# Kernel optimization log

Hardware: AMD Instinct MI355X
Metric: run time of the kernel (lower is better)

## Reference

```python
import jax, jax.numpy as jnp
import numpy as np

MAX_EMBED = 1024
MAX_HEADS = 16
MIN_WIDTH_RATIO = 0.25


def setup_inputs() -> dict:
    key = jax.random.key(0)
    ks = jax.random.split(key, 10)
    B, S, E = 4, 1024, MAX_EMBED
    query = jax.random.normal(ks[0], (B, S, E), dtype=jnp.float32)
    attention_mask = jax.random.randint(ks[1], (B, 1, 1, S), 0, 2, dtype=jnp.int32)
    # SlimmableLinear params (max sizes); kaiming-ish scale ~ 1/sqrt(fan_in)
    scale = 1.0 / np.sqrt(E)
    def lin(kw, kb):
        w = jax.random.uniform(kw, (E, E), dtype=jnp.float32, minval=-scale, maxval=scale)
        b = jax.random.uniform(kb, (E,), dtype=jnp.float32, minval=-scale, maxval=scale)
        return w, b
    q_w, q_b = lin(ks[2], ks[3])
    k_w, k_b = lin(ks[4], ks[5])
    v_w, v_b = lin(ks[6], ks[7])
    o_w, o_b = lin(ks[8], ks[9])
    return {"query": query, "attention_mask": attention_mask,
            "q_w": q_w, "q_b": q_b, "k_w": k_w, "k_b": k_b,
            "v_w": v_w, "v_b": v_b, "o_w": o_w, "o_b": o_b,
            "width": 768}


def _slim_linear(x, w, b, width):
    # weight stored [out, in] like torch; slice to [width, width]
    return x[..., :width] @ w[:width, :width].T + b[:width]


def reference(query, attention_mask, q_w, q_b, k_w, k_b, v_w, v_b, o_w, o_b, width):
    min_width = int(MAX_EMBED * MIN_WIDTH_RATIO)
    width = max(min_width, min(int(width), MAX_EMBED))
    num_heads = max(1, width * MAX_HEADS // MAX_EMBED)
    head_dim = width // num_heads
    B, S, _ = query.shape

    q = _slim_linear(query, q_w, q_b, width)  # [B,S,width]
    k = _slim_linear(query, k_w, k_b, width)  # key=query (self-attn)
    v = _slim_linear(query, v_w, v_b, width)

    q = q.reshape(B, S, num_heads, head_dim).transpose(0, 2, 1, 3)  # [B,H,S,D]
    k = k.reshape(B, S, num_heads, head_dim).transpose(0, 2, 1, 3)
    v = v.reshape(B, S, num_heads, head_dim).transpose(0, 2, 1, 3)

    scores = jnp.einsum('bhqd,bhkd->bhqk', q, k) / jnp.sqrt(jnp.float32(head_dim))
    scores = jnp.where(attention_mask == 0, jnp.float32(-1e9), scores)
    attn_weights = jax.nn.softmax(scores, axis=-1)  # [B,H,S,S]
    attn_output = jnp.einsum('bhqk,bhkd->bhqd', attn_weights, v)
    attn_output = attn_output.transpose(0, 2, 1, 3).reshape(B, S, width)
    output = attn_output @ o_w[:width, :width].T + o_b[:width]
    return output, attn_weights
```

## Files before the change

kernel.cpp:

```cpp
#include <hip/hip_runtime.h>

#define Bn 4
#define Sn 1024
#define En 1024
#define Wn 768
#define Hn 12
#define Dn 64
#define XE ((size_t)Bn * Sn * Wn)

typedef __attribute__((ext_vector_type(8))) short short8;
typedef __attribute__((ext_vector_type(4))) short short4v;
typedef __attribute__((ext_vector_type(4))) float floatx4;

#define MFMA16(A, B, C) __builtin_amdgcn_mfma_f32_16x16x32_bf16(A, B, C, 0, 0, 0)

__device__ __forceinline__ unsigned short f2bf_rn(float f) {
    unsigned int u = __float_as_uint(f);
    unsigned int r = u + 0x7fffu + ((u >> 16) & 1u);
    return (unsigned short)(r >> 16);
}
__device__ __forceinline__ float bf2f(unsigned short h) {
    return __uint_as_float(((unsigned int)h) << 16);
}

__device__ __forceinline__ void gload_lds16(const unsigned short* g, unsigned short* l) {
    __builtin_amdgcn_global_load_lds(
        (const __attribute__((address_space(1))) void*)g,
        (__attribute__((address_space(3))) void*)l, 16, 0, 0);
}

__global__ __launch_bounds__(256) void prep_kernel(
    const float* __restrict__ x,
    const float* __restrict__ qw, const float* __restrict__ kw,
    const float* __restrict__ vw, const float* __restrict__ ow,
    const float* __restrict__ qb, const float* __restrict__ kb,
    const float* __restrict__ vb,
    unsigned short* __restrict__ xh, unsigned short* __restrict__ xl,
    unsigned short* __restrict__ wqh, unsigned short* __restrict__ wql,
    unsigned short* __restrict__ woh, unsigned short* __restrict__ wol,
    float* __restrict__ bq)
{
    const int bx = blockIdx.x;
    const float* src; unsigned short *dh, *dl; int e;
    bool lo = true;
    if (bx < 3072) {
        e = (bx * 256 + threadIdx.x) * 4;
        src = x; dh = xh; dl = xl; lo = false;
    } else if (bx < 3072 + 1728) {
        int bb = bx - 3072; int which = bb / 576;
        e = ((bb - which * 576) * 256 + threadIdx.x) * 4;
        src = (which == 0) ? qw : (which == 1) ? kw : vw;
        dh = wqh + (size_t)which * Wn * Wn;
        dl = wql + (size_t)which * Wn * Wn;
    } else if (bx < 3072 + 1728 + 576) {
        e = ((bx - 3072 - 1728) * 256 + threadIdx.x) * 4;
        src = ow; dh = woh; dl = wol;
    } else {
        int t = (bx - 3072 - 1728 - 576) * 256 + threadIdx.x;
        if (t < Wn) bq[t] = qb[t];
        else if (t < 2 * Wn) bq[t] = kb[t - Wn];
        else if (t < 3 * Wn) bq[t] = vb[t - 2 * Wn];
        return;
    }
    int row = e / Wn, col = e - row * Wn;
    float4 v = *(const float4*)(src + (size_t)row * En + col);
    float f[4] = {v.x, v.y, v.z, v.w};
    short4v h, l;
    #pragma unroll
    for (int i = 0; i < 4; ++i) {
        unsigned short hh = f2bf_rn(f[i]);
        h[i] = (short)hh;
        l[i] = (short)f2bf_rn(f[i] - bf2f(hh));
    }
    *(short4v*)(dh + e) = h;
    if (lo) *(short4v*)(dl + e) = l;
}

__global__ __launch_bounds__(256) void qkv_mfma_kernel(
    const unsigned short* __restrict__ xh,
    const unsigned short* __restrict__ wh, const unsigned short* __restrict__ wl,
    const float* __restrict__ bq,
    unsigned short* __restrict__ qh_o, unsigned short* __restrict__ kh_o,
    unsigned short* __restrict__ vt_o)
{
    __shared__ __align__(16) unsigned short Ah[128 * 32];
    __shared__ __align__(16) unsigned short Bh[128 * 32];
    __shared__ __align__(16) unsigned short Bl[128 * 32];

    const int tid = threadIdx.x;
    const int wave = tid >> 6, lane = tid & 63;
    const int quad = lane >> 4, l16 = lane & 15;
    const int yy = ((int)blockIdx.y + 12) % 18;
    const int m0 = blockIdx.x * 128, n0 = yy * 128;
    const int wm = wave >> 1, wn = wave & 1;
    const int which = n0 / Wn;
    const bool full = (which == 2);

    floatx4 acc[4][4] = {};

    const int r_in = lane >> 2;
    const int cs = (lane & 3) ^ (r_in & 3);

    for (int k0 = 0; k0 < Wn; k0 += 32) {
        if (wave == 0) {
            #pragma unroll
            for (int i = 0; i < 8; ++i)
                gload_lds16(xh + (size_t)(m0 + i * 16 + r_in) * Wn + k0 + cs * 8,
                            Ah + i * 512);
        } else if (wave == 1) {
            #pragma unroll
            for (int i = 0; i < 8; ++i)
                gload_lds16(wh + (size_t)(n0 + i * 16 + r_in) * Wn + k0 + cs * 8,
                            Bh + i * 512);
        } else if (wave == 2 && full) {
            #pragma unroll
            for (int i = 0; i < 8; ++i)
                gload_lds16(wl + (size_t)(n0 + i * 16 + r_in) * Wn + k0 + cs * 8,
                            Bl + i * 512);
        }
        __syncthreads();

        short8 afh[4], bfh[4], bfl[4];
        #pragma unroll
        for (int t = 0; t < 4; ++t) {
            int mr = wm * 64 + t * 16 + l16;
            int ca = quad ^ (mr & 3);
            afh[t] = *(const short8*)(Ah + mr * 32 + ca * 8);
            int nr = wn * 64 + t * 16 + l16;
            int cb = quad ^ (nr & 3);
            bfh[t] = *(const short8*)(Bh + nr * 32 + cb * 8);
            if (full) bfl[t] = *(const short8*)(Bl + nr * 32 + cb * 8);
        }
        #pragma unroll
        for (int mt = 0; mt < 4; ++mt)
            #pragma unroll
            for (int nt = 0; nt < 4; ++nt) {
                acc[mt][nt] = MFMA16(afh[mt], bfh[nt], acc[mt][nt]);
                if (full) acc[mt][nt] = MFMA16(afh[mt], bfl[nt], acc[mt][nt]);
            }
        __syncthreads();
    }

    const int b = m0 >> 10;
    #pragma unroll
    for (int nt = 0; nt < 4; ++nt) {
        const int ng = n0 + wn * 64 + nt * 16 + l16;
        const float bias = bq[ng];
        const int f = ng - which * Wn;
        const int h = f >> 6, d = f & 63;
        #pragma unroll
        for (int mt = 0; mt < 4; ++mt) {
            const int mbase = m0 + wm * 64 + mt * 16 + quad * 4;
            const int s0 = mbase & (Sn - 1);
            if (which < 2) {
                unsigned short* oq = which ? kh_o : qh_o;
                size_t idx = (((size_t)(b * Hn + h)) * Sn + s0) * Dn + d;
                #pragma unroll
                for (int r = 0; r < 4; ++r)
                    oq[idx + (size_t)r * Dn] = f2bf_rn(acc[mt][nt][r] + bias);
            } else {
                size_t idx = (((size_t)(b * Hn + h)) * Dn + d) * Sn + s0;
                short4v pk;
                #pragma unroll
                for (int r = 0; r < 4; ++r)
                    pk[r] = (short)f2bf_rn(acc[mt][nt][r] + bias);
                *(short4v*)(vt_o + idx) = pk;
            }
        }
    }
}

__global__ __launch_bounds__(256) void attn_fused_kernel(
    const unsigned short* __restrict__ qh, const unsigned short* __restrict__ kh,
    const unsigned short* __restrict__ vt, const int* __restrict__ mask,
    float* __restrict__ attn,
    unsigned short* __restrict__ aoh, unsigned short* __restrict__ aol)
{
    __shared__ __align__(16) char PsObuf[3 * 16 * 68 * 4];
    __shared__ float msk[Sn];
    __shared__ float Lsum[4][16];

    unsigned short (*Ps)[16 * 72] =
        (unsigned short (*)[16 * 72])PsObuf;
    float (*Obuf)[16][68] = (float (*)[16][68])PsObuf;

    const int tid = threadIdx.x;
    const int wave = tid >> 6, lane = tid & 63;
    const int quad = lane >> 4, l16 = lane & 15;
    const int qt = blockIdx.x;
    const int h = blockIdx.y, b = blockIdx.z;
    const int bh = b * Hn + h;
    const size_t kvb = (size_t)bh * Sn * Dn;
    const size_t vbase = (size_t)bh * Dn * Sn;

    {
        int4 mi = *(const int4*)(mask + b * Sn + tid * 4);
        msk[tid * 4 + 0] = (float)mi.x;
        msk[tid * 4 + 1] = (float)mi.y;
        msk[tid * 4 + 2] = (float)mi.z;
        msk[tid * 4 + 3] = (float)mi.w;
    }

    const int qrow = qt * 16 + l16;
    short8 qf[2];
    {
        const unsigned short* qp = qh + kvb + (size_t)qrow * Dn + quad * 8;
        qf[0] = *(const short8*)(qp);
        qf[1] = *(const short8*)(qp + 32);
    }
    __syncthreads();

    short8 Pr[8];
    float lsumr[4] = {0.f, 0.f, 0.f, 0.f};
    const int kbase = wave * 256;

    #pragma unroll
    for (int kk = 0; kk < 4; ++kk) {
        const int k0 = kbase + kk * 64;
        #pragma unroll
        for (int ct = 0; ct < 4; ++ct) {
            const int key = k0 + ct * 16 + l16;
            const unsigned short* kp = kh + kvb + (size_t)key * Dn + quad * 8;
            short8 kf0 = *(const short8*)(kp);
            short8 kf1 = *(const short8*)(kp + 32);
            floatx4 acc = {0.f, 0.f, 0.f, 0.f};
            acc = MFMA16(qf[0], kf0, acc);
            acc = MFMA16(qf[1], kf1, acc);
            const float mv = msk[key];
            #pragma unroll
            for (int r = 0; r < 4; ++r) {
                const float e = __expf(acc[r] * 0.125f) * mv;
                lsumr[r] += e;
                Ps[wave][(quad * 4 + r) * 72 + ct * 16 + l16] = f2bf_rn(e);
            }
        }
        Pr[kk * 2 + 0] = *(const short8*)&Ps[wave][l16 * 72 + quad * 8];
        Pr[kk * 2 + 1] = *(const short8*)&Ps[wave][l16 * 72 + 32 + quad * 8];
    }

    #pragma unroll
    for (int r = 0; r < 4; ++r) {
        float v = lsumr[r];
        v += __shfl_xor(v, 1, 64);
        v += __shfl_xor(v, 2, 64);
        v += __shfl_xor(v, 4, 64);
        v += __shfl_xor(v, 8, 64);
        lsumr[r] = v;
    }
    if (l16 == 0) {
        #pragma unroll
        for (int r = 0; r < 4; ++r) Lsum[wave][quad * 4 + r] = lsumr[r];
    }
    __syncthreads();

    float li[4];
    #pragma unroll
    for (int r = 0; r < 4; ++r) {
        const float lv = Lsum[0][quad * 4 + r] + Lsum[1][quad * 4 + r]
                       + Lsum[2][quad * 4 + r] + Lsum[3][quad * 4 + r];
        li[r] = (lv > 0.f) ? 1.f / lv : 0.f;
    }
    float lt;
    {
        const float lv = Lsum[0][l16] + Lsum[1][l16] + Lsum[2][l16] + Lsum[3][l16];
        lt = (lv > 0.f) ? 1.f / lv : 0.f;
    }

    floatx4 oacc[4] = {};
    float* aprow = attn + ((size_t)bh * Sn + qrow) * Sn;

    #pragma unroll
    for (int kk = 0; kk < 4; ++kk) {
        const int k0 = kbase + kk * 64;
        #pragma unroll
        for (int ksp = 0; ksp < 2; ++ksp) {
            const short8 pf = Pr[kk * 2 + ksp];
            float4 f0, f1;
            f0.x = bf2f((unsigned short)pf[0]) * lt;
            f0.y = bf2f((unsigned short)pf[1]) * lt;
            f0.z = bf2f((unsigned short)pf[2]) * lt;
            f0.w = bf2f((unsigned short)pf[3]) * lt;
            f1.x = bf2f((unsigned short)pf[4]) * lt;
            f1.y = bf2f((unsigned short)pf[5]) * lt;
            f1.z = bf2f((unsigned short)pf[6]) * lt;
            f1.w = bf2f((unsigned short)pf[7]) * lt;
            float* ap = aprow + k0 + ksp * 32 + quad * 8;
            *(float4*)(ap)     = f0;
            *(float4*)(ap + 4) = f1;
            #pragma unroll
            for (int dt = 0; dt < 4; ++dt) {
                short8 vf = *(const short8*)(vt + vbase
                              + (size_t)(dt * 16 + l16) * Sn + k0 + ksp * 32 + quad * 8);
                oacc[dt] = MFMA16(pf, vf, oacc[dt]);
            }
        }
    }

    if (wave != 0) {
        #pragma unroll
        for (int dt = 0; dt < 4; ++dt)
            #pragma unroll
            for (int r = 0; r < 4; ++r)
                Obuf[wave - 1][quad * 4 + r][dt * 16 + l16] = oacc[dt][r];
    }
    __syncthreads();
    if (wave == 0) {
        const int row0 = qt * 16 + quad * 4;
        #pragma unroll
        for (int dt = 0; dt < 4; ++dt)
            #pragma unroll
            for (int r = 0; r < 4; ++r) {
                const float o = (oacc[dt][r]
                               + Obuf[0][quad * 4 + r][dt * 16 + l16]
                               + Obuf[1][quad * 4 + r][dt * 16 + l16]
                               + Obuf[2][quad * 4 + r][dt * 16 + l16]) * li[r];
                const unsigned short hh = f2bf_rn(o);
                const size_t idx = ((size_t)b * Sn + row0 + r) * Wn + h * Dn + dt * 16 + l16;
                aoh[idx] = hh;
                aol[idx] = f2bf_rn(o - bf2f(hh));
            }
    }
}

__global__ __launch_bounds__(256) void oproj_mfma_kernel(
    const unsigned short* __restrict__ aoh, const unsigned short* __restrict__ aol,
    const unsigned short* __restrict__ wh, const unsigned short* __restrict__ wl,
    const float* __restrict__ ob, float* __restrict__ out)
{
    __shared__ __align__(16) unsigned short Ah[64 * 32];
    __shared__ __align__(16) unsigned short Al[64 * 32];
    __shared__ __align__(16) unsigned short Bh[128 * 32];
    __shared__ __align__(16) unsigned short Bl[128 * 32];

    const int tid = threadIdx.x;
    const int wave = tid >> 6, lane = tid & 63;
    const int quad = lane >> 4, l16 = lane & 15;
    const int m0 = blockIdx.x * 64, n0 = blockIdx.y * 128;
    const int wm = wave >> 1, wn = wave & 1;

    floatx4 acc[2][4] = {};

    const int r_in = lane >> 2;
    const int cs = (lane & 3) ^ (r_in & 3);

    for (int k0 = 0; k0 < Wn; k0 += 32) {
        if (wave == 0) {
            #pragma unroll
            for (int i = 0; i < 4; ++i) {
                gload_lds16(aoh + (size_t)(m0 + i * 16 + r_in) * Wn + k0 + cs * 8,
                            Ah + i * 512);
                gload_lds16(aol + (size_t)(m0 + i * 16 + r_in) * Wn + k0 + cs * 8,
                            Al + i * 512);
            }
        } else if (wave == 1) {
            #pragma unroll
            for (int i = 0; i < 8; ++i)
                gload_lds16(wh + (size_t)(n0 + i * 16 + r_in) * Wn + k0 + cs * 8,
                            Bh + i * 512);
        } else if (wave == 2) {
            #pragma unroll
            for (int i = 0; i < 8; ++i)
                gload_lds16(wl + (size_t)(n0 + i * 16 + r_in) * Wn + k0 + cs * 8,
                            Bl + i * 512);
        }
        __syncthreads();

        short8 afh[2], afl[2], bfh[4], bfl[4];
        #pragma unroll
        for (int t = 0; t < 2; ++t) {
            int mr = wm * 32 + t * 16 + l16;
            int ca = quad ^ (mr & 3);
            afh[t] = *(const short8*)(Ah + mr * 32 + ca * 8);
            afl[t] = *(const short8*)(Al + mr * 32 + ca * 8);
        }
        #pragma unroll
        for (int t = 0; t < 4; ++t) {
            int nr = wn * 64 + t * 16 + l16;
            int cb = quad ^ (nr & 3);
            bfh[t] = *(const short8*)(Bh + nr * 32 + cb * 8);
            bfl[t] = *(const short8*)(Bl + nr * 32 + cb * 8);
        }
        #pragma unroll
        for (int mt = 0; mt < 2; ++mt)
            #pragma unroll
            for (int nt = 0; nt < 4; ++nt) {
                acc[mt][nt] = MFMA16(afh[mt], bfh[nt], acc[mt][nt]);
                acc[mt][nt] = MFMA16(afh[mt], bfl[nt], acc[mt][nt]);
                acc[mt][nt] = MFMA16(afl[mt], bfh[nt], acc[mt][nt]);
            }
        __syncthreads();
    }

    #pragma unroll
    for (int nt = 0; nt < 4; ++nt) {
        const int ng = n0 + wn * 64 + nt * 16 + l16;
        const float bias = ob[ng];
        #pragma unroll
        for (int mt = 0; mt < 2; ++mt) {
            const int m = m0 + wm * 32 + mt * 16 + quad * 4;
            #pragma unroll
            for (int r = 0; r < 4; ++r)
                out[(size_t)(m + r) * Wn + ng] = acc[mt][nt][r] + bias;
        }
    }
}

extern "C" void kernel_launch(void* const* d_in, const int* in_sizes, int n_in,
                              void* d_out, int out_size, void* d_ws, size_t ws_size,
                              hipStream_t stream) {
    const float* x    = (const float*)d_in[0];
    const int*   mask = (const int*)  d_in[1];
    const float* qw = (const float*)d_in[2];
    const float* qb = (const float*)d_in[3];
    const float* kw = (const float*)d_in[4];
    const float* kb = (const float*)d_in[5];
    const float* vw = (const float*)d_in[6];
    const float* vb = (const float*)d_in[7];
    const float* ow = (const float*)d_in[8];
    const float* ob = (const float*)d_in[9];

    float* out  = (float*)d_out;
    float* attn = out + XE;

    char* w = (char*)d_ws;
    unsigned short* xh   = (unsigned short*)w;  w += XE * 2;
    unsigned short* xl   = (unsigned short*)w;  w += XE * 2;
    unsigned short* wqh  = (unsigned short*)w;  w += (size_t)3 * Wn * Wn * 2;
    unsigned short* wql  = (unsigned short*)w;  w += (size_t)3 * Wn * Wn * 2;
    unsigned short* woh  = (unsigned short*)w;  w += (size_t)Wn * Wn * 2;
    unsigned short* wol  = (unsigned short*)w;  w += (size_t)Wn * Wn * 2;
    float*          bq   = (float*)w;           w += (size_t)3 * Wn * 4;
    unsigned short* qh   = (unsigned short*)w;  w += XE * 2;
    unsigned short* kh   = (unsigned short*)w;  w += XE * 2;
    unsigned short* vt_w = (unsigned short*)w;  w += XE * 2;

    prep_kernel<<<5385, 256, 0, stream>>>(x, qw, kw, vw, ow, qb, kb, vb,
                                          xh, xl, wqh, wql, woh, wol, bq);

    qkv_mfma_kernel<<<dim3(32, 18), 256, 0, stream>>>(
        xh, wqh, wql, bq, qh, kh, vt_w);

    attn_fused_kernel<<<dim3(64, Hn, Bn), 256, 0, stream>>>(
        qh, kh, vt_w, mask, attn, xh, xl);

    oproj_mfma_kernel<<<dim3(64, 6), 256, 0, stream>>>(
        xh, xl, woh, wol, ob, out);
}
```

Measured before the change: 384.1 us.

## Stage attention-prob stores through LDS and drop low-bf16 split for O-projection input

Result: faster. 374.4 us (-2.5%).

```diff
diff --git a/kernel.cpp b/kernel.cpp
--- a/kernel.cpp
+++ b/kernel.cpp
@@ -52,6 +52,7 @@
         src = (which == 0) ? qw : (which == 1) ? kw : vw;
         dh = wqh + (size_t)which * Wn * Wn;
         dl = wql + (size_t)which * Wn * Wn;
+        lo = (which == 2);
     } else if (bx < 3072 + 1728 + 576) {
         e = ((bx - 3072 - 1728) * 256 + threadIdx.x) * 4;
         src = ow; dh = woh; dl = wol;
@@ -173,15 +174,15 @@
 __global__ __launch_bounds__(256) void attn_fused_kernel(
     const unsigned short* __restrict__ qh, const unsigned short* __restrict__ kh,
     const unsigned short* __restrict__ vt, const int* __restrict__ mask,
-    float* __restrict__ attn,
-    unsigned short* __restrict__ aoh, unsigned short* __restrict__ aol)
+    float* __restrict__ attn, unsigned short* __restrict__ aoh)
 {
-    __shared__ __align__(16) char PsObuf[3 * 16 * 68 * 4];
+    __shared__ __align__(16) char PsObuf[4 * 16 * 68 * 4];
     __shared__ float msk[Sn];
     __shared__ float Lsum[4][16];
 
     unsigned short (*Ps)[16 * 72] =
         (unsigned short (*)[16 * 72])PsObuf;
+    float (*PsF)[16][68] = (float (*)[16][68])PsObuf;
     float (*Obuf)[16][68] = (float (*)[16][68])PsObuf;
 
     const int tid = threadIdx.x;
@@ -267,7 +268,7 @@
     }
 
     floatx4 oacc[4] = {};
-    float* aprow = attn + ((size_t)bh * Sn + qrow) * Sn;
+    float* abase = attn + ((size_t)bh * Sn + qt * 16) * Sn;
 
     #pragma unroll
     for (int kk = 0; kk < 4; ++kk) {
@@ -284,9 +285,8 @@
             f1.y = bf2f((unsigned short)pf[5]) * lt;
             f1.z = bf2f((unsigned short)pf[6]) * lt;
             f1.w = bf2f((unsigned short)pf[7]) * lt;
-            float* ap = aprow + k0 + ksp * 32 + quad * 8;
-            *(float4*)(ap)     = f0;
-            *(float4*)(ap + 4) = f1;
+            *(float4*)&PsF[wave][l16][ksp * 32 + quad * 8]     = f0;
+            *(float4*)&PsF[wave][l16][ksp * 32 + quad * 8 + 4] = f1;
             #pragma unroll
             for (int dt = 0; dt < 4; ++dt) {
                 short8 vf = *(const short8*)(vt + vbase
@@ -294,8 +294,14 @@
                 oacc[dt] = MFMA16(pf, vf, oacc[dt]);
             }
         }
-    }
-
+        #pragma unroll
+        for (int rb = 0; rb < 4; ++rb) {
+            float4 v4 = *(const float4*)&PsF[wave][rb * 4 + quad][l16 * 4];
+            *(float4*)(abase + (size_t)(rb * 4 + quad) * Sn + k0 + l16 * 4) = v4;
+        }
+    }
+
+    __syncthreads();
     if (wave != 0) {
         #pragma unroll
         for (int dt = 0; dt < 4; ++dt)
@@ -314,21 +320,18 @@
                                + Obuf[0][quad * 4 + r][dt * 16 + l16]
                                + Obuf[1][quad * 4 + r][dt * 16 + l16]
                                + Obuf[2][quad * 4 + r][dt * 16 + l16]) * li[r];
-                const unsigned short hh = f2bf_rn(o);
                 const size_t idx = ((size_t)b * Sn + row0 + r) * Wn + h * Dn + dt * 16 + l16;
-                aoh[idx] = hh;
-                aol[idx] = f2bf_rn(o - bf2f(hh));
+                aoh[idx] = f2bf_rn(o);
             }
     }
 }
 
 __global__ __launch_bounds__(256) void oproj_mfma_kernel(
-    const unsigned short* __restrict__ aoh, const unsigned short* __restrict__ aol,
+    const unsigned short* __restrict__ aoh,
     const unsigned short* __restrict__ wh, const unsigned short* __restrict__ wl,
     const float* __restrict__ ob, float* __restrict__ out)
 {
     __shared__ __align__(16) unsigned short Ah[64 * 32];
-    __shared__ __align__(16) unsigned short Al[64 * 32];
     __shared__ __align__(16) unsigned short Bh[128 * 32];
     __shared__ __align__(16) unsigned short Bl[128 * 32];
 
@@ -346,12 +349,9 @@
     for (int k0 = 0; k0 < Wn; k0 += 32) {
         if (wave == 0) {
             #pragma unroll
-            for (int i = 0; i < 4; ++i) {
+            for (int i = 0; i < 4; ++i)
                 gload_lds16(aoh + (size_t)(m0 + i * 16 + r_in) * Wn + k0 + cs * 8,
                             Ah + i * 512);
-                gload_lds16(aol + (size_t)(m0 + i * 16 + r_in) * Wn + k0 + cs * 8,
-                            Al + i * 512);
-            }
         } else if (wave == 1) {
             #pragma unroll
             for (int i = 0; i < 8; ++i)
@@ -365,13 +365,12 @@
         }
         __syncthreads();
 
-        short8 afh[2], afl[2], bfh[4], bfl[4];
+        short8 afh[2], bfh[4], bfl[4];
         #pragma unroll
         for (int t = 0; t < 2; ++t) {
             int mr = wm * 32 + t * 16 + l16;
             int ca = quad ^ (mr & 3);
             afh[t] = *(const short8*)(Ah + mr * 32 + ca * 8);
-            afl[t] = *(const short8*)(Al + mr * 32 + ca * 8);
         }
         #pragma unroll
         for (int t = 0; t < 4; ++t) {
@@ -386,7 +385,6 @@
             for (int nt = 0; nt < 4; ++nt) {
                 acc[mt][nt] = MFMA16(afh[mt], bfh[nt], acc[mt][nt]);
                 acc[mt][nt] = MFMA16(afh[mt], bfl[nt], acc[mt][nt]);
-                acc[mt][nt] = MFMA16(afl[mt], bfh[nt], acc[mt][nt]);
             }
         __syncthreads();
     }
@@ -441,8 +439,8 @@
         xh, wqh, wql, bq, qh, kh, vt_w);
 
     attn_fused_kernel<<<dim3(64, Hn, Bn), 256, 0, stream>>>(
-        qh, kh, vt_w, mask, attn, xh, xl);
+        qh, kh, vt_w, mask, attn, xh);
 
     oproj_mfma_kernel<<<dim3(64, 6), 256, 0, stream>>>(
-        xh, xl, woh, wol, ob, out);
-}
+        xh, woh, wol, ob, out);
+}
```
